# Kernel tuning notes

Measured on AMD Instinct MI355X. Metric: run time of the kernel, lower is better.

Reference implementation:

```python
import jax, jax.numpy as jnp
import numpy as np

# --- sizes / simulation constants (match init_kwargs) ---
IN_F, OUT_F, BIAS = 512, 512, 1
BATCH = 128
RES, SIM_TIME, TAU_SYN = 1e-4, 2e-2, 5e-3
STEPS = int(np.ceil(SIM_TIME / RES))                 # 200
DECAY_SYN = float(np.exp(-RES / TAU_SYN))
DECAY_MEM = float(np.exp(-RES / TAU_SYN))            # original code uses tau_syn for both


def setup_inputs() -> dict:
    key = jax.random.key(0)
    k1, k2, k3, k4 = jax.random.split(key, 4)
    # input spikes inside the first half of the sim window
    input_times = jax.random.uniform(k1, (BATCH, IN_F), jnp.float32) * (0.5 * SIM_TIME)
    # weights_init = (0.05, 0.1) normal
    weights = 0.05 + 0.1 * jax.random.normal(k2, (IN_F + BIAS, OUT_F), jnp.float32)
    # delays_init = (0.001, 0.0005) normal, kept non-negative
    delays = jnp.abs(0.001 + 0.0005 * jax.random.normal(k3, (IN_F + BIAS, OUT_F), jnp.float32))
    # thresholds_init = (1.0, 0.05) normal
    thresholds = 1.0 + 0.05 * jax.random.normal(k4, (OUT_F,), jnp.float32)
    return {"input_times": input_times, "weights": weights,
            "delays": delays, "thresholds": thresholds}


def _snn_forward(input_times, weights, delays, thresholds):
    B = input_times.shape[0]
    dt = input_times.dtype
    # bias inputs spike at t = 0
    times = jnp.concatenate([input_times, jnp.zeros((B, BIAS), dt)], axis=1)   # [B, I+bias]
    # per-synapse delayed arrival times -> time-step indices
    arrival = times[:, :, None] + delays[None]                                  # [B, I+bias, O]
    step_idx = jnp.clip(jnp.round(arrival / RES).astype(jnp.int32), 0, STEPS - 1)
    b_idx = jnp.arange(B)[:, None, None]
    o_idx = jnp.arange(OUT_F)[None, None, :]
    w = jnp.broadcast_to(weights[None], arrival.shape)
    # charge[b, t, o] = sum_i w[i,o] * 1[arrival step of synapse (i,o) == t]
    charge = jnp.zeros((B, STEPS, OUT_F), dt).at[b_idx, step_idx, o_idx].add(w)
    charge = jnp.moveaxis(charge, 1, 0)                                         # [steps, B, O]

    thr = thresholds[None]                                                      # [1, O]

    def body(carry, inp):
        syn, mem, spike_t, spiked = carry
        t, c = inp
        syn_n = syn * DECAY_SYN + c
        mem_n = mem * DECAY_MEM + (1.0 - DECAY_MEM) * syn_n
        crossing = jnp.logical_and(~spiked, mem_n >= thr)
        denom = mem_n - mem
        safe = jnp.where(jnp.abs(denom) > 1e-12, denom, 1e-12)
        frac = jnp.clip((thr - mem) / safe, 0.0, 1.0)     # linear interp inside the step
        t_cross = (t + frac) * RES
        spike_t = jnp.where(crossing, t_cross, spike_t)
        spiked = jnp.logical_or(spiked, crossing)
        return (syn_n, mem_n, spike_t, spiked), None

    init = (jnp.zeros((B, OUT_F), dt),
            jnp.zeros((B, OUT_F), dt),
            jnp.full((B, OUT_F), SIM_TIME, dt),           # "no spike" -> sim_time
            jnp.zeros((B, OUT_F), bool))
    ts = jnp.arange(STEPS, dtype=dt)
    (syn, mem, spike_t, spiked), _ = jax.lax.scan(body, init, (ts, charge))
    return spike_t                                        # [B, O] first-spike times


def reference(input_times, weights, delays, thresholds):
    return _snn_forward(input_times, weights, delays, thresholds)
```

## Files before the change

### kernel.cpp

```cpp
#include <hip/hip_runtime.h>


#define IN_F    512
#define OUT_F   512
#define BATCH   128
#define STEPS   200
#define RES_F   1e-4f
#define CSTRIDE 65
#define DECAY_F 0.98019867330675525f
#define ONEMD_F 0.019801326693244747f
#define SIM_T_F 2e-2f
#define FPSCALE 8388608.0f
#define INVSCALE 1.1920928955078125e-07f

__device__ __forceinline__ int bin_of(float arr) {
    float q = (float)((double)arr * 10000.0);
    int s = __float2int_rn(q);
    return s > STEPS - 1 ? STEPS - 1 : s;
}

__global__ __launch_bounds__(512, 4) void snn_fwd(
    const float* __restrict__ input_times,
    const float* __restrict__ weights,
    const float* __restrict__ delays,
    const float* __restrict__ thresholds,
    float* __restrict__ out)
{
#pragma clang fp contract(off)
    __shared__ __align__(16) int chargeI[STEPS * CSTRIDE];
    __shared__ float times_s[IN_F];

    const int tid  = threadIdx.x;
    const int wv   = tid >> 6;
    const int lane = tid & 63;
    const int b     = blockIdx.x >> 3;
    const int otile = blockIdx.x & 7;
    const int ob    = otile << 6;

    {
        int4 z = make_int4(0, 0, 0, 0);
        int4* c4 = (int4*)chargeI;
        #pragma unroll
        for (int k = tid; k < (STEPS * CSTRIDE) / 4; k += 512) c4[k] = z;
    }
    times_s[tid] = input_times[b * IN_F + tid];
    __syncthreads();

    const int sub = lane >> 4;
    const int cg  = (lane & 15) << 2;
    const float4* __restrict__ Wp = (const float4*)weights;
    const float4* __restrict__ Dp = (const float4*)delays;
    const int r0   = wv << 6;
    const int i0   = (r0 + sub) * (OUT_F / 4) + ((ob + cg) >> 2);
    const int gstr = 4 * (OUT_F / 4);

    if (wv == 7) {
        float dl = delays[IN_F * OUT_F + ob + lane];
        int   wt = __float2int_rn(weights[IN_F * OUT_F + ob + lane] * FPSCALE);
        atomicAdd(&chargeI[bin_of(dl) * CSTRIDE + lane], wt);
    }

    float4 wA = Wp[i0],            wB = Wp[i0 + gstr];
    float4 dA = Dp[i0],            dB = Dp[i0 + gstr];
    float  tA = times_s[r0 + sub];
    float  tB = times_s[r0 + 4 + sub];

    #pragma unroll
    for (int g = 0; g < 16; g += 2) {
        float4 wC = {}, wD = {};
        float4 dC = {}, dD = {};
        float  tC = 0.f, tD = 0.f;
        if (g + 2 < 16) {
            wC = Wp[i0 + (g + 2) * gstr]; dC = Dp[i0 + (g + 2) * gstr];
            tC = times_s[r0 + ((g + 2) << 2) + sub];
        }
        if (g + 3 < 16) {
            wD = Wp[i0 + (g + 3) * gstr]; dD = Dp[i0 + (g + 3) * gstr];
            tD = times_s[r0 + ((g + 3) << 2) + sub];
        }
        {
            const float* dv = (const float*)&dA;
            const float* wf = (const float*)&wA;
            #pragma unroll
            for (int k = 0; k < 4; ++k) {
                int s  = bin_of(tA + dv[k]);
                int wt = __float2int_rn(wf[k] * FPSCALE);
                atomicAdd(&chargeI[s * CSTRIDE + cg + k], wt);
            }
        }
        {
            const float* dv = (const float*)&dB;
            const float* wf = (const float*)&wB;
            #pragma unroll
            for (int k = 0; k < 4; ++k) {
                int s  = bin_of(tB + dv[k]);
                int wt = __float2int_rn(wf[k] * FPSCALE);
                atomicAdd(&chargeI[s * CSTRIDE + cg + k], wt);
            }
        }
        wA = wC; dA = dC; tA = tC;
        wB = wD; dB = dD; tB = tD;
    }
    __syncthreads();

    if (wv == 0) {
        const float thr = thresholds[ob + lane];
        float syn = 0.f, mem = 0.f, spike_t = SIM_T_F;
        bool spiked = false;
        for (int t0 = 0; t0 < STEPS; t0 += 4) {
            float c[4];
            #pragma unroll
            for (int j = 0; j < 4; ++j)
                c[j] = (float)chargeI[(t0 + j) * CSTRIDE + lane] * INVSCALE;
            #pragma unroll
            for (int j = 0; j < 4; ++j) {
                float syn_n = syn * DECAY_F + c[j];
                float mem_n = mem * DECAY_F + ONEMD_F * syn_n;
                if (!spiked && mem_n >= thr) {
                    float denom = mem_n - mem;
                    float safe  = fabsf(denom) > 1e-12f ? denom : 1e-12f;
                    float frac  = (thr - mem) / safe;
                    frac = frac < 0.f ? 0.f : (frac > 1.f ? 1.f : frac);
                    spike_t = ((float)(t0 + j) + frac) * RES_F;
                    spiked  = true;
                }
                syn = syn_n; mem = mem_n;
            }
            if (__all(spiked)) break;
        }
        out[b * OUT_F + ob + lane] = spike_t;
    }
}

extern "C" void kernel_launch(void* const* d_in, const int* in_sizes, int n_in,
                              void* d_out, int out_size, void* d_ws, size_t ws_size,
                              hipStream_t stream) {
    const float* input_times = (const float*)d_in[0];
    const float* weights     = (const float*)d_in[1];
    const float* delays      = (const float*)d_in[2];
    const float* thresholds  = (const float*)d_in[3];
    float* out = (float*)d_out;
    (void)d_ws; (void)ws_size;

    dim3 grid(BATCH * (OUT_F / 64));
    snn_fwd<<<grid, 512, 0, stream>>>(input_times, weights, delays,
                                      thresholds, out);
}
```

Before: 77.79 us.

## Process two batch rows per block to reuse weight and delay loads

Each block now handles two batch rows and 32 output columns instead of one row and 64 columns. Every weight/delay float4 loaded from global memory then feeds atomics into two shared charge histograms, which halves per-block global traffic per unit of work. The scan phase packs both batch rows into one 64-lane wave. In exchange there are more atomics per thread, the charge stride shrinks to 33, and a 32-wide column tile may give less coalesced reads and more shared-atomic contention per column.

Result: faster. 76.26 us (-2.0%).

```diff
diff --git a/kernel.cpp b/kernel.cpp
--- a/kernel.cpp
+++ b/kernel.cpp
@@ -6,7 +6,7 @@
 #define BATCH   128
 #define STEPS   200
 #define RES_F   1e-4f
-#define CSTRIDE 65
+#define CSTRIDE 33
 #define DECAY_F 0.98019867330675525f
 #define ONEMD_F 0.019801326693244747f
 #define SIM_T_F 2e-2f
@@ -27,65 +27,69 @@
     float* __restrict__ out)
 {
 #pragma clang fp contract(off)
-    __shared__ __align__(16) int chargeI[STEPS * CSTRIDE];
-    __shared__ float times_s[IN_F];
+    __shared__ __align__(16) int chargeI[2][STEPS * CSTRIDE];
+    __shared__ float times_s[2][IN_F];
 
     const int tid  = threadIdx.x;
     const int wv   = tid >> 6;
     const int lane = tid & 63;
-    const int b     = blockIdx.x >> 3;
-    const int otile = blockIdx.x & 7;
-    const int ob    = otile << 6;
+    const int b0    = (blockIdx.x >> 4) << 1;
+    const int otile = blockIdx.x & 15;
+    const int ob    = otile << 5;
 
     {
         int4 z = make_int4(0, 0, 0, 0);
-        int4* c4 = (int4*)chargeI;
-        #pragma unroll
-        for (int k = tid; k < (STEPS * CSTRIDE) / 4; k += 512) c4[k] = z;
+        int4* c4 = (int4*)&chargeI[0][0];
+        for (int k = tid; k < (2 * STEPS * CSTRIDE) / 4; k += 512) c4[k] = z;
     }
-    times_s[tid] = input_times[b * IN_F + tid];
+    times_s[0][tid] = input_times[b0 * IN_F + tid];
+    times_s[1][tid] = input_times[(b0 + 1) * IN_F + tid];
     __syncthreads();
 
-    const int sub = lane >> 4;
-    const int cg  = (lane & 15) << 2;
+    const int sub = lane >> 3;
+    const int cgi = lane & 7;
+    const int cg  = cgi << 2;
     const float4* __restrict__ Wp = (const float4*)weights;
     const float4* __restrict__ Dp = (const float4*)delays;
     const int r0   = wv << 6;
-    const int i0   = (r0 + sub) * (OUT_F / 4) + ((ob + cg) >> 2);
-    const int gstr = 4 * (OUT_F / 4);
+    const int i0   = (r0 + sub) * (OUT_F / 4) + (ob >> 2) + cgi;
+    const int gstr = 8 * (OUT_F / 4);
 
     if (wv == 7) {
-        float dl = delays[IN_F * OUT_F + ob + lane];
-        int   wt = __float2int_rn(weights[IN_F * OUT_F + ob + lane] * FPSCALE);
-        atomicAdd(&chargeI[bin_of(dl) * CSTRIDE + lane], wt);
+        const int bt = lane >> 5, col = lane & 31;
+        float dl = delays[IN_F * OUT_F + ob + col];
+        int   wt = __float2int_rn(weights[IN_F * OUT_F + ob + col] * FPSCALE);
+        atomicAdd(&chargeI[bt][bin_of(dl) * CSTRIDE + col], wt);
     }
 
     float4 wA = Wp[i0],            wB = Wp[i0 + gstr];
     float4 dA = Dp[i0],            dB = Dp[i0 + gstr];
-    float  tA = times_s[r0 + sub];
-    float  tB = times_s[r0 + 4 + sub];
+    float  tA0 = times_s[0][r0 + sub],     tA1 = times_s[1][r0 + sub];
+    float  tB0 = times_s[0][r0 + 8 + sub], tB1 = times_s[1][r0 + 8 + sub];
 
     #pragma unroll
-    for (int g = 0; g < 16; g += 2) {
+    for (int g = 0; g < 8; g += 2) {
         float4 wC = {}, wD = {};
         float4 dC = {}, dD = {};
-        float  tC = 0.f, tD = 0.f;
-        if (g + 2 < 16) {
+        float  tC0 = 0.f, tC1 = 0.f, tD0 = 0.f, tD1 = 0.f;
+        if (g + 2 < 8) {
             wC = Wp[i0 + (g + 2) * gstr]; dC = Dp[i0 + (g + 2) * gstr];
-            tC = times_s[r0 + ((g + 2) << 2) + sub];
+            tC0 = times_s[0][r0 + ((g + 2) << 3) + sub];
+            tC1 = times_s[1][r0 + ((g + 2) << 3) + sub];
         }
-        if (g + 3 < 16) {
+        if (g + 3 < 8) {
             wD = Wp[i0 + (g + 3) * gstr]; dD = Dp[i0 + (g + 3) * gstr];
-            tD = times_s[r0 + ((g + 3) << 2) + sub];
+            tD0 = times_s[0][r0 + ((g + 3) << 3) + sub];
+            tD1 = times_s[1][r0 + ((g + 3) << 3) + sub];
         }
         {
             const float* dv = (const float*)&dA;
             const float* wf = (const float*)&wA;
             #pragma unroll
             for (int k = 0; k < 4; ++k) {
-                int s  = bin_of(tA + dv[k]);
                 int wt = __float2int_rn(wf[k] * FPSCALE);
-                atomicAdd(&chargeI[s * CSTRIDE + cg + k], wt);
+                atomicAdd(&chargeI[0][bin_of(tA0 + dv[k]) * CSTRIDE + cg + k], wt);
+                atomicAdd(&chargeI[1][bin_of(tA1 + dv[k]) * CSTRIDE + cg + k], wt);
             }
         }
         {
@@ -93,25 +97,26 @@
             const float* wf = (const float*)&wB;
             #pragma unroll
             for (int k = 0; k < 4; ++k) {
-                int s  = bin_of(tB + dv[k]);
                 int wt = __float2int_rn(wf[k] * FPSCALE);
-                atomicAdd(&chargeI[s * CSTRIDE + cg + k], wt);
+                atomicAdd(&chargeI[0][bin_of(tB0 + dv[k]) * CSTRIDE + cg + k], wt);
+                atomicAdd(&chargeI[1][bin_of(tB1 + dv[k]) * CSTRIDE + cg + k], wt);
             }
         }
-        wA = wC; dA = dC; tA = tC;
-        wB = wD; dB = dD; tB = tD;
+        wA = wC; dA = dC; tA0 = tC0; tA1 = tC1;
+        wB = wD; dB = dD; tB0 = tD0; tB1 = tD1;
     }
     __syncthreads();
 
     if (wv == 0) {
-        const float thr = thresholds[ob + lane];
+        const int bt = lane >> 5, col = lane & 31;
+        const float thr = thresholds[ob + col];
         float syn = 0.f, mem = 0.f, spike_t = SIM_T_F;
         bool spiked = false;
         for (int t0 = 0; t0 < STEPS; t0 += 4) {
             float c[4];
             #pragma unroll
             for (int j = 0; j < 4; ++j)
-                c[j] = (float)chargeI[(t0 + j) * CSTRIDE + lane] * INVSCALE;
+                c[j] = (float)chargeI[bt][(t0 + j) * CSTRIDE + col] * INVSCALE;
             #pragma unroll
             for (int j = 0; j < 4; ++j) {
                 float syn_n = syn * DECAY_F + c[j];
@@ -128,7 +133,7 @@
             }
             if (__all(spiked)) break;
         }
-        out[b * OUT_F + ob + lane] = spike_t;
+        out[(b0 + bt) * OUT_F + ob + col] = spike_t;
     }
 }
 
@@ -142,7 +147,7 @@
     float* out = (float*)d_out;
     (void)d_ws; (void)ws_size;
 
-    dim3 grid(BATCH * (OUT_F / 64));
+    dim3 grid((BATCH / 2) * (OUT_F / 32));
     snn_fwd<<<grid, 512, 0, stream>>>(input_times, weights, delays,
                                       thresholds, out);
 }
```
